# Kernel optimization log

Measured on AMD Instinct MI355X. Metric: run time of the kernel, lower is better.

Reference implementation:

```python
import jax, jax.numpy as jnp
import numpy as np

LAYERS = [3, 256, 256, 256, 256, 256, 256, 3]
W_BC, W_DIV, W_JXB = 1.0, 1.0, 1.0  # weight1 = [1.0, 1.0, 1.0]


def setup_inputs() -> dict:
    key = jax.random.key(0)
    ks = jax.random.split(key, 32)
    N0, NF = 16384, 32768
    inp = {
        "x0": jax.random.uniform(ks[0], (N0, 1), jnp.float32),
        "y0": jax.random.uniform(ks[1], (N0, 1), jnp.float32),
        "bx0": jax.random.normal(ks[2], (N0, 1), jnp.float32),
        "by0": jax.random.normal(ks[3], (N0, 1), jnp.float32),
        "bz0": jax.random.normal(ks[4], (N0, 1), jnp.float32),
        "xyz_f": jax.random.uniform(ks[5], (NF, 3), jnp.float32),
        "lb": jnp.zeros((3,), jnp.float32),
        "ub": jnp.ones((3,), jnp.float32),
    }
    # Xavier-normal weights, zero biases (as in initialize_NN)
    for l in range(len(LAYERS) - 1):
        fan_in, fan_out = LAYERS[l], LAYERS[l + 1]
        std = (2.0 / (fan_in + fan_out)) ** 0.5
        inp[f"W{l}"] = std * jax.random.normal(ks[6 + l], (fan_in, fan_out), jnp.float32)
        inp[f"b{l}"] = jnp.zeros((1, fan_out), jnp.float32)
    return inp


def reference(x0, y0, bx0, by0, bz0, xyz_f, lb, ub,
              W0, b0, W1, b1, W2, b2, W3, b3, W4, b4, W5, b5, W6, b6):
    Ws = [W0, W1, W2, W3, W4, W5, W6]
    bs = [b0, b1, b2, b3, b4, b5, b6]

    def net(p):  # p: (3,) -> (3,) field [bx, by, bz]
        h = 2.0 * (p - lb) / (ub - lb) - 1.0
        for W, b in zip(Ws[:-1], bs[:-1]):
            h = jnp.tanh(h @ W + b[0])
        return h @ Ws[-1] + bs[-1][0]

    # Boundary term at z = 0
    pts0 = jnp.concatenate([x0, y0, jnp.zeros_like(x0)], axis=1)  # (N0, 3)
    b_bc = jax.vmap(net)(pts0)  # (N0, 3)

    # One fused forward-mode pass gives the full 3x3 Jacobian + primal,
    # replacing the 9 separate autograd.grad sweeps of the torch code.
    def val_and_jac(p):
        primal, jac = jax.vmap(lambda t: jax.jvp(net, (p,), (t,)))(jnp.eye(3, dtype=p.dtype))
        return primal[0], jac  # jac[j, i] = d b_i / d x_j

    bf, jac = jax.vmap(val_and_jac)(xyz_f)  # (NF, 3), (NF, 3, 3)

    div = jac[:, 0, 0] + jac[:, 1, 1] + jac[:, 2, 2]  # bx_x + by_y + bz_z
    bx, by, bz = bf[:, 0], bf[:, 1], bf[:, 2]
    jx = jac[:, 1, 2] - jac[:, 2, 1]  # bz_y - by_z
    jy = jac[:, 2, 0] - jac[:, 0, 2]  # bx_z - bz_x
    jz = jac[:, 0, 1] - jac[:, 1, 0]  # by_x - bx_y
    jxb = (jy * bz - jz * by) ** 2 + (jz * bx - jx * bz) ** 2 + (jx * by - jy * bx) ** 2

    loss = (W_BC * jnp.mean((b_bc[:, 0:1] - bx0) ** 2)
            + W_BC * jnp.mean((b_bc[:, 1:2] - by0) ** 2)
            + W_BC * jnp.mean((b_bc[:, 2:3] - bz0) ** 2)
            + W_DIV * jnp.mean(div ** 2)
            + W_JXB * jnp.mean(jxb))
    return loss
```

## Files before the change

kernel.cpp:

```cpp
#include <hip/hip_runtime.h>
#include <math.h>

typedef short bf16x8 __attribute__((ext_vector_type(8)));
typedef short bf16x4 __attribute__((ext_vector_type(4)));
typedef float f32x4 __attribute__((ext_vector_type(4)));

#define NPT0 16384
#define NPTF 32768

__device__ __forceinline__ short f2b(float f) {
  union { float f; unsigned u; } v; v.f = f;
  return (short)((v.u + 0x7FFFu + ((v.u >> 16) & 1u)) >> 16);
}
__device__ __forceinline__ int cvtpk(float a, float b) {
  int r;
  asm("v_cvt_pk_bf16_f32 %0, %1, %2" : "=v"(r) : "v"(a), "v"(b));
  return r;
}
__device__ __forceinline__ float tanh_fast(float z) {
  const float e = __expf(2.f * z);
  return 1.f - 2.f * __builtin_amdgcn_rcpf(e + 1.f);
}


__global__ void prep_kernel(const float* __restrict__ W1, const float* __restrict__ W2,
                            const float* __restrict__ W3, const float* __restrict__ W4,
                            const float* __restrict__ W5, const float* __restrict__ W6,
                            short* __restrict__ Wt)
{
  const int i = blockIdx.x * 256 + threadIdx.x;
  if (i < 5 * 65536) {
    const int layer = i >> 16;
    const float* src = layer == 0 ? W1 : layer == 1 ? W2 : layer == 2 ? W3
                     : layer == 3 ? W4 : W5;
    const int w  = i & 65535;
    const int nt = w >> 12;
    const int ks = (w >> 9) & 7;
    const int l  = (w >> 3) & 63;
    const int e  = w & 7;
    const int n  = nt * 16 + (l & 15);
    const int k  = ks * 32 + (l >> 4) * 8 + e;
    Wt[i] = f2b(src[k * 256 + n]);
  } else {
    const int w  = i - 5 * 65536;
    const int ks = w >> 9;
    const int l  = (w >> 3) & 63;
    const int e  = w & 7;
    const int n  = l & 15;
    const int k  = ks * 32 + (l >> 4) * 8 + e;
    Wt[i] = (n < 3) ? f2b(W6[k * 3 + n]) : (short)0;
  }
}

__global__ __launch_bounds__(256, 3) void field_kernel(
    const float* __restrict__ xyz_f,
    const float* __restrict__ lb, const float* __restrict__ ub,
    const float* __restrict__ W0, const float* __restrict__ b0,
    const float* __restrict__ b1, const float* __restrict__ b2,
    const float* __restrict__ b3, const float* __restrict__ b4,
    const float* __restrict__ b5,
    const short* __restrict__ Wt,
    const float* __restrict__ b6,
    float* __restrict__ part_div2, float* __restrict__ part_jxb)
{
  __shared__ short act[4 * 4096];
  __shared__ float redD[192];
  const int tid = threadIdx.x;
  const int lane = tid & 63;
  const int wv = tid >> 6;
  const int c = lane & 15;
  const int kg = lane >> 4;
  const int nbase = wv * 64;

  const float lbx = lb[0], lby = lb[1], lbz = lb[2];
  const float sx = 2.f / (ub[0] - lbx);
  const float sy = 2.f / (ub[1] - lby);
  const float sz = 2.f / (ub[2] - lbz);

  {
    const int p = tid >> 4;
    const int pt = blockIdx.x * 16 + p;
    const int n0 = (tid & 15) * 16;
    const float hx = (xyz_f[pt * 3 + 0] - lbx) * sx - 1.f;
    const float hy = (xyz_f[pt * 3 + 1] - lby) * sy - 1.f;
    const float hz = (xyz_f[pt * 3 + 2] - lbz) * sz - 1.f;
    float th[16], vx[16], vy[16], vz[16];
#pragma unroll
    for (int j = 0; j < 16; ++j) {
      const int n = n0 + j;
      const float w0 = W0[n], w1 = W0[256 + n], w2 = W0[512 + n];
      const float z = b0[n] + hx * w0 + hy * w1 + hz * w2;
      const float t = tanh_fast(z);
      const float g = 1.f - t * t;
      th[j] = t;
      vx[j] = g * sx * w0;
      vy[j] = g * sy * w1;
      vz[j] = g * sz * w2;
    }
    const int ks0 = n0 >> 5;
    const int kgb = (n0 >> 3) & 3;
#pragma unroll
    for (int half = 0; half < 2; ++half) {
      const int j0 = half * 8;
      const int idx = ks0 * 512 + ((kgb + half) * 16 + p) * 8;
      int4 o0, o1, o2, o3;
      o0.x = cvtpk(th[j0+0], th[j0+1]); o0.y = cvtpk(th[j0+2], th[j0+3]);
      o0.z = cvtpk(th[j0+4], th[j0+5]); o0.w = cvtpk(th[j0+6], th[j0+7]);
      o1.x = cvtpk(vx[j0+0], vx[j0+1]); o1.y = cvtpk(vx[j0+2], vx[j0+3]);
      o1.z = cvtpk(vx[j0+4], vx[j0+5]); o1.w = cvtpk(vx[j0+6], vx[j0+7]);
      o2.x = cvtpk(vy[j0+0], vy[j0+1]); o2.y = cvtpk(vy[j0+2], vy[j0+3]);
      o2.z = cvtpk(vy[j0+4], vy[j0+5]); o2.w = cvtpk(vy[j0+6], vy[j0+7]);
      o3.x = cvtpk(vz[j0+0], vz[j0+1]); o3.y = cvtpk(vz[j0+2], vz[j0+3]);
      o3.z = cvtpk(vz[j0+4], vz[j0+5]); o3.w = cvtpk(vz[j0+6], vz[j0+7]);
      *(int4*)&act[idx]          = o0;
      *(int4*)&act[4096 + idx]   = o1;
      *(int4*)&act[8192 + idx]   = o2;
      *(int4*)&act[12288 + idx]  = o3;
    }
  }
  __syncthreads();

  const float* const bsArr[5] = {b1, b2, b3, b4, b5};

#pragma unroll
  for (int layer = 0; layer < 5; ++layer) {
    const short* wt0 = Wt + layer * 65536 + wv * 4 * 4096 + lane * 8;
    const short* wt1 = wt0 + 4096;
    const short* wt2 = wt0 + 8192;
    const short* wt3 = wt0 + 12288;

    f32x4 acc[4][4];
#pragma unroll
    for (int s = 0; s < 4; ++s)
#pragma unroll
      for (int t = 0; t < 4; ++t) acc[s][t] = (f32x4){0.f, 0.f, 0.f, 0.f};

#pragma unroll
    for (int ks = 0; ks < 8; ++ks) {
      const int sa = ks * 512 + lane * 8;
      const bf16x8 a0 = *(const bf16x8*)&act[sa];
      const bf16x8 a1 = *(const bf16x8*)&act[4096 + sa];
      const bf16x8 a2 = *(const bf16x8*)&act[8192 + sa];
      const bf16x8 a3 = *(const bf16x8*)&act[12288 + sa];
      const bf16x8 w0 = *(const bf16x8*)(wt0 + ks * 512);
      const bf16x8 w1 = *(const bf16x8*)(wt1 + ks * 512);
      const bf16x8 w2 = *(const bf16x8*)(wt2 + ks * 512);
      const bf16x8 w3 = *(const bf16x8*)(wt3 + ks * 512);
      acc[0][0] = __builtin_amdgcn_mfma_f32_16x16x32_bf16(w0, a0, acc[0][0], 0, 0, 0);
      acc[1][0] = __builtin_amdgcn_mfma_f32_16x16x32_bf16(w0, a1, acc[1][0], 0, 0, 0);
      acc[2][0] = __builtin_amdgcn_mfma_f32_16x16x32_bf16(w0, a2, acc[2][0], 0, 0, 0);
      acc[3][0] = __builtin_amdgcn_mfma_f32_16x16x32_bf16(w0, a3, acc[3][0], 0, 0, 0);
      acc[0][1] = __builtin_amdgcn_mfma_f32_16x16x32_bf16(w1, a0, acc[0][1], 0, 0, 0);
      acc[1][1] = __builtin_amdgcn_mfma_f32_16x16x32_bf16(w1, a1, acc[1][1], 0, 0, 0);
      acc[2][1] = __builtin_amdgcn_mfma_f32_16x16x32_bf16(w1, a2, acc[2][1], 0, 0, 0);
      acc[3][1] = __builtin_amdgcn_mfma_f32_16x16x32_bf16(w1, a3, acc[3][1], 0, 0, 0);
      acc[0][2] = __builtin_amdgcn_mfma_f32_16x16x32_bf16(w2, a0, acc[0][2], 0, 0, 0);
      acc[1][2] = __builtin_amdgcn_mfma_f32_16x16x32_bf16(w2, a1, acc[1][2], 0, 0, 0);
      acc[2][2] = __builtin_amdgcn_mfma_f32_16x16x32_bf16(w2, a2, acc[2][2], 0, 0, 0);
      acc[3][2] = __builtin_amdgcn_mfma_f32_16x16x32_bf16(w2, a3, acc[3][2], 0, 0, 0);
      acc[0][3] = __builtin_amdgcn_mfma_f32_16x16x32_bf16(w3, a0, acc[0][3], 0, 0, 0);
      acc[1][3] = __builtin_amdgcn_mfma_f32_16x16x32_bf16(w3, a1, acc[1][3], 0, 0, 0);
      acc[2][3] = __builtin_amdgcn_mfma_f32_16x16x32_bf16(w3, a2, acc[2][3], 0, 0, 0);
      acc[3][3] = __builtin_amdgcn_mfma_f32_16x16x32_bf16(w3, a3, acc[3][3], 0, 0, 0);
    }
    __syncthreads();

    const float* bl = bsArr[layer];
#pragma unroll
    for (int t = 0; t < 4; ++t) {
      const int n0 = nbase + t * 16 + kg * 4;
      const f32x4 bias = *(const f32x4*)(bl + n0);
      float th[4], g[4];
#pragma unroll
      for (int r = 0; r < 4; ++r) {
        th[r] = tanh_fast(acc[0][t][r] + bias[r]);
        g[r] = 1.f - th[r] * th[r];
      }
      int2 o0, o1, o2, o3;
      o0.x = cvtpk(th[0], th[1]);
      o0.y = cvtpk(th[2], th[3]);
      o1.x = cvtpk(g[0] * acc[1][t][0], g[1] * acc[1][t][1]);
      o1.y = cvtpk(g[2] * acc[1][t][2], g[3] * acc[1][t][3]);
      o2.x = cvtpk(g[0] * acc[2][t][0], g[1] * acc[2][t][1]);
      o2.y = cvtpk(g[2] * acc[2][t][2], g[3] * acc[2][t][3]);
      o3.x = cvtpk(g[0] * acc[3][t][0], g[1] * acc[3][t][1]);
      o3.y = cvtpk(g[2] * acc[3][t][2], g[3] * acc[3][t][3]);
      const int idx = (n0 >> 5) * 512 + (((n0 >> 3) & 3) * 16 + c) * 8 + (n0 & 7);
      *(int2*)&act[idx]         = o0;
      *(int2*)&act[4096 + idx]  = o1;
      *(int2*)&act[8192 + idx]  = o2;
      *(int2*)&act[12288 + idx] = o3;
    }
    __syncthreads();
  }

  {
    const short* w6 = Wt + 5 * 65536 + lane * 8;
    f32x4 accT = (f32x4){0.f, 0.f, 0.f, 0.f};
#pragma unroll
    for (int ks = 0; ks < 8; ++ks) {
      const bf16x8 w = *(const bf16x8*)(w6 + ks * 512);
      const bf16x8 b = *(const bf16x8*)&act[wv * 4096 + ks * 512 + lane * 8];
      accT = __builtin_amdgcn_mfma_f32_16x16x32_bf16(w, b, accT, 0, 0, 0);
    }
    if (kg == 0) {
      redD[wv * 48 + 0  + c] = accT[0];
      redD[wv * 48 + 16 + c] = accT[1];
      redD[wv * 48 + 32 + c] = accT[2];
    }
  }
  __syncthreads();
  if (tid < 16) {
    const int p = tid;
    const float bx = redD[0 + p]  + b6[0];
    const float by = redD[16 + p] + b6[1];
    const float bz = redD[32 + p] + b6[2];
    const float j00 = redD[48 + p],  j01 = redD[64 + p],  j02 = redD[80 + p];
    const float j10 = redD[96 + p],  j11 = redD[112 + p], j12 = redD[128 + p];
    const float j20 = redD[144 + p], j21 = redD[160 + p], j22 = redD[176 + p];
    const float dv = j00 + j11 + j22;
    const float jx = j12 - j21;
    const float jy = j20 - j02;
    const float jz = j01 - j10;
    const float e1 = jy * bz - jz * by;
    const float e2 = jz * bx - jx * bz;
    const float e3 = jx * by - jy * bx;
    float d2 = dv * dv;
    float jb = e1 * e1 + e2 * e2 + e3 * e3;
#pragma unroll
    for (int m = 1; m < 16; m <<= 1) {
      d2 += __shfl_xor(d2, m);
      jb += __shfl_xor(jb, m);
    }
    if (tid == 0) {
      part_div2[blockIdx.x] = d2;
      part_jxb[blockIdx.x]  = jb;
    }
  }
}

__global__ __launch_bounds__(256, 4) void bc_kernel(
    const float* __restrict__ x0, const float* __restrict__ y0,
    const float* __restrict__ bx0, const float* __restrict__ by0,
    const float* __restrict__ bz0,
    const float* __restrict__ lb, const float* __restrict__ ub,
    const float* __restrict__ W0, const float* __restrict__ b0,
    const float* __restrict__ b1, const float* __restrict__ b2,
    const float* __restrict__ b3, const float* __restrict__ b4,
    const float* __restrict__ b5,
    const short* __restrict__ Wt,
    const float* __restrict__ b6,
    float* __restrict__ part_bc)
{
  __shared__ short act[4096];
  const int tid = threadIdx.x;
  const int lane = tid & 63;
  const int wv = tid >> 6;
  const int c = lane & 15;
  const int kg = lane >> 4;
  const int nbase = wv * 64;

  const float lbx = lb[0], lby = lb[1], lbz = lb[2];
  const float sx = 2.f / (ub[0] - lbx);
  const float sy = 2.f / (ub[1] - lby);
  const float sz = 2.f / (ub[2] - lbz);

  {
    const int p = tid >> 4;
    const int pt = blockIdx.x * 16 + p;
    const int n0 = (tid & 15) * 16;
    const float hx = (x0[pt] - lbx) * sx - 1.f;
    const float hy = (y0[pt] - lby) * sy - 1.f;
    const float hz = (0.f - lbz) * sz - 1.f;
    float th[16];
#pragma unroll
    for (int j = 0; j < 16; ++j) {
      const int n = n0 + j;
      const float z = b0[n] + hx * W0[n] + hy * W0[256 + n] + hz * W0[512 + n];
      th[j] = tanh_fast(z);
    }
    const int ks0 = n0 >> 5;
    const int kgb = (n0 >> 3) & 3;
#pragma unroll
    for (int half = 0; half < 2; ++half) {
      const int j0 = half * 8;
      int4 o;
      o.x = cvtpk(th[j0+0], th[j0+1]); o.y = cvtpk(th[j0+2], th[j0+3]);
      o.z = cvtpk(th[j0+4], th[j0+5]); o.w = cvtpk(th[j0+6], th[j0+7]);
      *(int4*)&act[ks0 * 512 + ((kgb + half) * 16 + p) * 8] = o;
    }
  }
  __syncthreads();

  const float* const bsArr[5] = {b1, b2, b3, b4, b5};

#pragma unroll
  for (int layer = 0; layer < 5; ++layer) {
    const short* wt0 = Wt + layer * 65536 + wv * 4 * 4096 + lane * 8;

    bf16x8 a[8];
#pragma unroll
    for (int ks = 0; ks < 8; ++ks) a[ks] = *(const bf16x8*)&act[ks * 512 + lane * 8];
    __syncthreads();

    f32x4 acc[4];
#pragma unroll
    for (int t = 0; t < 4; ++t) acc[t] = (f32x4){0.f, 0.f, 0.f, 0.f};

#pragma unroll
    for (int ks = 0; ks < 8; ++ks) {
#pragma unroll
      for (int t = 0; t < 4; ++t) {
        const bf16x8 w = *(const bf16x8*)(wt0 + t * 4096 + ks * 512);
        acc[t] = __builtin_amdgcn_mfma_f32_16x16x32_bf16(w, a[ks], acc[t], 0, 0, 0);
      }
    }

    const float* bl = bsArr[layer];
#pragma unroll
    for (int t = 0; t < 4; ++t) {
      const int n0 = nbase + t * 16 + kg * 4;
      const f32x4 bias = *(const f32x4*)(bl + n0);
      float th[4];
#pragma unroll
      for (int r = 0; r < 4; ++r) th[r] = tanh_fast(acc[t][r] + bias[r]);
      int2 o;
      o.x = cvtpk(th[0], th[1]);
      o.y = cvtpk(th[2], th[3]);
      const int idx = (n0 >> 5) * 512 + (((n0 >> 3) & 3) * 16 + c) * 8 + (n0 & 7);
      *(int2*)&act[idx] = o;
    }
    __syncthreads();
  }

  if (wv == 0) {
    const short* w6 = Wt + 5 * 65536 + lane * 8;
    f32x4 accT = (f32x4){0.f, 0.f, 0.f, 0.f};
#pragma unroll
    for (int ks = 0; ks < 8; ++ks) {
      const bf16x8 w = *(const bf16x8*)(w6 + ks * 512);
      const bf16x8 b = *(const bf16x8*)&act[ks * 512 + lane * 8];
      accT = __builtin_amdgcn_mfma_f32_16x16x32_bf16(w, b, accT, 0, 0, 0);
    }
    if (lane < 16) {
      const int pt = blockIdx.x * 16 + lane;
      const float ex = accT[0] + b6[0] - bx0[pt];
      const float ey = accT[1] + b6[1] - by0[pt];
      const float ez = accT[2] + b6[2] - bz0[pt];
      float abc = ex * ex + ey * ey + ez * ez;
#pragma unroll
      for (int m = 1; m < 16; m <<= 1) abc += __shfl_xor(abc, m);
      if (lane == 0) part_bc[blockIdx.x] = abc;
    }
  }
}

__global__ void reduce_kernel(const float* __restrict__ parts, float* __restrict__ out)
{
  __shared__ float sdata[12];
  const int tid = threadIdx.x, lane = tid & 63, wv = tid >> 6;
  float d = 0.f, j = 0.f, b = 0.f;
  for (int i = tid; i < 2048; i += 256) { d += parts[i]; j += parts[2048 + i]; }
  for (int i = tid; i < 1024; i += 256) b += parts[4096 + i];
  for (int off = 32; off > 0; off >>= 1) {
    d += __shfl_down(d, off);
    j += __shfl_down(j, off);
    b += __shfl_down(b, off);
  }
  if (lane == 0) {
    sdata[wv * 3 + 0] = d;
    sdata[wv * 3 + 1] = j;
    sdata[wv * 3 + 2] = b;
  }
  __syncthreads();
  if (tid == 0) {
    float sd = 0.f, sj = 0.f, sb = 0.f;
    for (int w = 0; w < 4; ++w) {
      sd += sdata[w * 3 + 0];
      sj += sdata[w * 3 + 1];
      sb += sdata[w * 3 + 2];
    }
    out[0] = sb / (float)NPT0 + sd / (float)NPTF + sj / (float)NPTF;
  }
}

extern "C" void kernel_launch(void* const* d_in, const int* in_sizes, int n_in,
                              void* d_out, int out_size, void* d_ws, size_t ws_size,
                              hipStream_t stream)
{
  const float* x0    = (const float*)d_in[0];
  const float* y0    = (const float*)d_in[1];
  const float* bx0   = (const float*)d_in[2];
  const float* by0   = (const float*)d_in[3];
  const float* bz0   = (const float*)d_in[4];
  const float* xyz_f = (const float*)d_in[5];
  const float* lb    = (const float*)d_in[6];
  const float* ub    = (const float*)d_in[7];
  const float* W0 = (const float*)d_in[8];
  const float* b0 = (const float*)d_in[9];
  const float* W1 = (const float*)d_in[10];
  const float* b1 = (const float*)d_in[11];
  const float* W2 = (const float*)d_in[12];
  const float* b2 = (const float*)d_in[13];
  const float* W3 = (const float*)d_in[14];
  const float* b3 = (const float*)d_in[15];
  const float* W4 = (const float*)d_in[16];
  const float* b4 = (const float*)d_in[17];
  const float* W5 = (const float*)d_in[18];
  const float* b5 = (const float*)d_in[19];
  const float* W6 = (const float*)d_in[20];
  const float* b6 = (const float*)d_in[21];

  short* Wt = (short*)d_ws;
  float* parts = (float*)((char*)d_ws + (5 * 65536 + 4096) * sizeof(short));
  float* p_div2 = parts;
  float* p_jxb  = parts + 2048;
  float* p_bc   = parts + 4096;

  prep_kernel<<<1296, 256, 0, stream>>>(W1, W2, W3, W4, W5, W6, Wt);
  field_kernel<<<2048, 256, 0, stream>>>(xyz_f, lb, ub, W0, b0,
      b1, b2, b3, b4, b5, Wt, b6, p_div2, p_jxb);
  bc_kernel<<<1024, 256, 0, stream>>>(x0, y0, bx0, by0, bz0, lb, ub, W0, b0,
      b1, b2, b3, b4, b5, Wt, b6, p_bc);
  reduce_kernel<<<1, 256, 0, stream>>>(parts, (float*)d_out);
}
```

Measured before the change: 127.5 us.

## Process 32 points per block with 8 waves splitting output columns

Doubles each block to 512 threads and 32 points, with each of the 8 waves computing 2 output column tiles across two 16-point groups instead of 4 tiles for one group. Every weight fragment loaded from global memory now feeds twice as many MFMAs, halving weight traffic per point and the number of blocks. The cost is a doubled LDS activation buffer, a re-indexed tail reduction, and different occupancy and register-pressure behaviour under the new launch bounds.

```diff
diff --git a/kernel.cpp b/kernel.cpp
--- a/kernel.cpp
+++ b/kernel.cpp
@@ -2,7 +2,6 @@
 #include <math.h>
 
 typedef short bf16x8 __attribute__((ext_vector_type(8)));
-typedef short bf16x4 __attribute__((ext_vector_type(4)));
 typedef float f32x4 __attribute__((ext_vector_type(4)));
 
 #define NPT0 16384
@@ -21,7 +20,9 @@
   const float e = __expf(2.f * z);
   return 1.f - 2.f * __builtin_amdgcn_rcpf(e + 1.f);
 }
-
+__device__ __forceinline__ int inplane(int n, int c) {
+  return ((n >> 5) << 9) + ((((n >> 3) & 3) * 16 + c) << 3) + (n & 7);
+}
 
 __global__ void prep_kernel(const float* __restrict__ W1, const float* __restrict__ W2,
                             const float* __restrict__ W3, const float* __restrict__ W4,
@@ -52,7 +53,7 @@
   }
 }
 
-__global__ __launch_bounds__(256, 3) void field_kernel(
+__global__ __launch_bounds__(512, 4) void field_kernel(
     const float* __restrict__ xyz_f,
     const float* __restrict__ lb, const float* __restrict__ ub,
     const float* __restrict__ W0, const float* __restrict__ b0,
@@ -63,14 +64,13 @@
     const float* __restrict__ b6,
     float* __restrict__ part_div2, float* __restrict__ part_jxb)
 {
-  __shared__ short act[4 * 4096];
-  __shared__ float redD[192];
+  __shared__ short act[4 * 8192];
+  __shared__ float redD[4 * 96];
   const int tid = threadIdx.x;
   const int lane = tid & 63;
   const int wv = tid >> 6;
   const int c = lane & 15;
   const int kg = lane >> 4;
-  const int nbase = wv * 64;
 
   const float lbx = lb[0], lby = lb[1], lbz = lb[2];
   const float sx = 2.f / (ub[0] - lbx);
@@ -78,9 +78,10 @@
   const float sz = 2.f / (ub[2] - lbz);
 
   {
-    const int p = tid >> 4;
-    const int pt = blockIdx.x * 16 + p;
-    const int n0 = (tid & 15) * 16;
+    const int pp = tid & 15;
+    const int pg = (tid >> 4) & 1;
+    const int pt = blockIdx.x * 32 + pg * 16 + pp;
+    const int n0 = (tid >> 5) * 16;
     const float hx = (xyz_f[pt * 3 + 0] - lbx) * sx - 1.f;
     const float hy = (xyz_f[pt * 3 + 1] - lby) * sy - 1.f;
     const float hz = (xyz_f[pt * 3 + 2] - lbz) * sz - 1.f;
@@ -102,7 +103,7 @@
 #pragma unroll
     for (int half = 0; half < 2; ++half) {
       const int j0 = half * 8;
-      const int idx = ks0 * 512 + ((kgb + half) * 16 + p) * 8;
+      const int idx = pg * 4096 + ks0 * 512 + ((kgb + half) * 16 + pp) * 8;
       int4 o0, o1, o2, o3;
       o0.x = cvtpk(th[j0+0], th[j0+1]); o0.y = cvtpk(th[j0+2], th[j0+3]);
       o0.z = cvtpk(th[j0+4], th[j0+5]); o0.w = cvtpk(th[j0+6], th[j0+7]);
@@ -113,9 +114,9 @@
       o3.x = cvtpk(vz[j0+0], vz[j0+1]); o3.y = cvtpk(vz[j0+2], vz[j0+3]);
       o3.z = cvtpk(vz[j0+4], vz[j0+5]); o3.w = cvtpk(vz[j0+6], vz[j0+7]);
       *(int4*)&act[idx]          = o0;
-      *(int4*)&act[4096 + idx]   = o1;
-      *(int4*)&act[8192 + idx]   = o2;
-      *(int4*)&act[12288 + idx]  = o3;
+      *(int4*)&act[8192 + idx]   = o1;
+      *(int4*)&act[16384 + idx]  = o2;
+      *(int4*)&act[24576 + idx]  = o3;
     }
   }
   __syncthreads();
@@ -124,100 +125,96 @@
 
 #pragma unroll
   for (int layer = 0; layer < 5; ++layer) {
-    const short* wt0 = Wt + layer * 65536 + wv * 4 * 4096 + lane * 8;
-    const short* wt1 = wt0 + 4096;
-    const short* wt2 = wt0 + 8192;
-    const short* wt3 = wt0 + 12288;
-
-    f32x4 acc[4][4];
-#pragma unroll
-    for (int s = 0; s < 4; ++s)
-#pragma unroll
-      for (int t = 0; t < 4; ++t) acc[s][t] = (f32x4){0.f, 0.f, 0.f, 0.f};
+    const short* wbase = Wt + layer * 65536 + (wv * 2) * 4096 + lane * 8;
+
+    f32x4 acc[2][4][2];
+#pragma unroll
+    for (int t = 0; t < 2; ++t)
+#pragma unroll
+      for (int s = 0; s < 4; ++s)
+#pragma unroll
+        for (int g = 0; g < 2; ++g) acc[t][s][g] = (f32x4){0.f, 0.f, 0.f, 0.f};
 
 #pragma unroll
     for (int ks = 0; ks < 8; ++ks) {
       const int sa = ks * 512 + lane * 8;
-      const bf16x8 a0 = *(const bf16x8*)&act[sa];
-      const bf16x8 a1 = *(const bf16x8*)&act[4096 + sa];
-      const bf16x8 a2 = *(const bf16x8*)&act[8192 + sa];
-      const bf16x8 a3 = *(const bf16x8*)&act[12288 + sa];
-      const bf16x8 w0 = *(const bf16x8*)(wt0 + ks * 512);
-      const bf16x8 w1 = *(const bf16x8*)(wt1 + ks * 512);
-      const bf16x8 w2 = *(const bf16x8*)(wt2 + ks * 512);
-      const bf16x8 w3 = *(const bf16x8*)(wt3 + ks * 512);
-      acc[0][0] = __builtin_amdgcn_mfma_f32_16x16x32_bf16(w0, a0, acc[0][0], 0, 0, 0);
-      acc[1][0] = __builtin_amdgcn_mfma_f32_16x16x32_bf16(w0, a1, acc[1][0], 0, 0, 0);
-      acc[2][0] = __builtin_amdgcn_mfma_f32_16x16x32_bf16(w0, a2, acc[2][0], 0, 0, 0);
-      acc[3][0] = __builtin_amdgcn_mfma_f32_16x16x32_bf16(w0, a3, acc[3][0], 0, 0, 0);
-      acc[0][1] = __builtin_amdgcn_mfma_f32_16x16x32_bf16(w1, a0, acc[0][1], 0, 0, 0);
-      acc[1][1] = __builtin_amdgcn_mfma_f32_16x16x32_bf16(w1, a1, acc[1][1], 0, 0, 0);
-      acc[2][1] = __builtin_amdgcn_mfma_f32_16x16x32_bf16(w1, a2, acc[2][1], 0, 0, 0);
-      acc[3][1] = __builtin_amdgcn_mfma_f32_16x16x32_bf16(w1, a3, acc[3][1], 0, 0, 0);
-      acc[0][2] = __builtin_amdgcn_mfma_f32_16x16x32_bf16(w2, a0, acc[0][2], 0, 0, 0);
-      acc[1][2] = __builtin_amdgcn_mfma_f32_16x16x32_bf16(w2, a1, acc[1][2], 0, 0, 0);
-      acc[2][2] = __builtin_amdgcn_mfma_f32_16x16x32_bf16(w2, a2, acc[2][2], 0, 0, 0);
-      acc[3][2] = __builtin_amdgcn_mfma_f32_16x16x32_bf16(w2, a3, acc[3][2], 0, 0, 0);
-      acc[0][3] = __builtin_amdgcn_mfma_f32_16x16x32_bf16(w3, a0, acc[0][3], 0, 0, 0);
-      acc[1][3] = __builtin_amdgcn_mfma_f32_16x16x32_bf16(w3, a1, acc[1][3], 0, 0, 0);
-      acc[2][3] = __builtin_amdgcn_mfma_f32_16x16x32_bf16(w3, a2, acc[2][3], 0, 0, 0);
-      acc[3][3] = __builtin_amdgcn_mfma_f32_16x16x32_bf16(w3, a3, acc[3][3], 0, 0, 0);
+      const bf16x8 w0 = *(const bf16x8*)(wbase + ks * 512);
+      const bf16x8 w1 = *(const bf16x8*)(wbase + 4096 + ks * 512);
+#pragma unroll
+      for (int g = 0; g < 2; ++g) {
+        const bf16x8 a0 = *(const bf16x8*)&act[g * 4096 + sa];
+        const bf16x8 a1 = *(const bf16x8*)&act[8192 + g * 4096 + sa];
+        const bf16x8 a2 = *(const bf16x8*)&act[16384 + g * 4096 + sa];
+        const bf16x8 a3 = *(const bf16x8*)&act[24576 + g * 4096 + sa];
+        acc[0][0][g] = __builtin_amdgcn_mfma_f32_16x16x32_bf16(w0, a0, acc[0][0][g], 0, 0, 0);
+        acc[0][1][g] = __builtin_amdgcn_mfma_f32_16x16x32_bf16(w0, a1, acc[0][1][g], 0, 0, 0);
+        acc[0][2][g] = __builtin_amdgcn_mfma_f32_16x16x32_bf16(w0, a2, acc[0][2][g], 0, 0, 0);
+        acc[0][3][g] = __builtin_amdgcn_mfma_f32_16x16x32_bf16(w0, a3, acc[0][3][g], 0, 0, 0);
+        acc[1][0][g] = __builtin_amdgcn_mfma_f32_16x16x32_bf16(w1, a0, acc[1][0][g], 0, 0, 0);
+        acc[1][1][g] = __builtin_amdgcn_mfma_f32_16x16x32_bf16(w1, a1, acc[1][1][g], 0, 0, 0);
+        acc[1][2][g] = __builtin_amdgcn_mfma_f32_16x16x32_bf16(w1, a2, acc[1][2][g], 0, 0, 0);
+        acc[1][3][g] = __builtin_amdgcn_mfma_f32_16x16x32_bf16(w1, a3, acc[1][3][g], 0, 0, 0);
+      }
     }
     __syncthreads();
 
     const float* bl = bsArr[layer];
 #pragma unroll
-    for (int t = 0; t < 4; ++t) {
-      const int n0 = nbase + t * 16 + kg * 4;
+    for (int t = 0; t < 2; ++t) {
+      const int n0 = (wv * 2 + t) * 16 + kg * 4;
       const f32x4 bias = *(const f32x4*)(bl + n0);
-      float th[4], g[4];
-#pragma unroll
-      for (int r = 0; r < 4; ++r) {
-        th[r] = tanh_fast(acc[0][t][r] + bias[r]);
-        g[r] = 1.f - th[r] * th[r];
+#pragma unroll
+      for (int g = 0; g < 2; ++g) {
+        float th[4], gd[4];
+#pragma unroll
+        for (int r = 0; r < 4; ++r) {
+          th[r] = tanh_fast(acc[t][0][g][r] + bias[r]);
+          gd[r] = 1.f - th[r] * th[r];
+        }
+        int2 o0, o1, o2, o3;
+        o0.x = cvtpk(th[0], th[1]);
+        o0.y = cvtpk(th[2], th[3]);
+        o1.x = cvtpk(gd[0] * acc[t][1][g][0], gd[1] * acc[t][1][g][1]);
+        o1.y = cvtpk(gd[2] * acc[t][1][g][2], gd[3] * acc[t][1][g][3]);
+        o2.x = cvtpk(gd[0] * acc[t][2][g][0], gd[1] * acc[t][2][g][1]);
+        o2.y = cvtpk(gd[2] * acc[t][2][g][2], gd[3] * acc[t][2][g][3]);
+        o3.x = cvtpk(gd[0] * acc[t][3][g][0], gd[1] * acc[t][3][g][1]);
+        o3.y = cvtpk(gd[2] * acc[t][3][g][2], gd[3] * acc[t][3][g][3]);
+        const int idx = g * 4096 + inplane(n0, c);
+        *(int2*)&act[idx]          = o0;
+        *(int2*)&act[8192 + idx]   = o1;
+        *(int2*)&act[16384 + idx]  = o2;
+        *(int2*)&act[24576 + idx]  = o3;
       }
-      int2 o0, o1, o2, o3;
-      o0.x = cvtpk(th[0], th[1]);
-      o0.y = cvtpk(th[2], th[3]);
-      o1.x = cvtpk(g[0] * acc[1][t][0], g[1] * acc[1][t][1]);
-      o1.y = cvtpk(g[2] * acc[1][t][2], g[3] * acc[1][t][3]);
-      o2.x = cvtpk(g[0] * acc[2][t][0], g[1] * acc[2][t][1]);
-      o2.y = cvtpk(g[2] * acc[2][t][2], g[3] * acc[2][t][3]);
-      o3.x = cvtpk(g[0] * acc[3][t][0], g[1] * acc[3][t][1]);
-      o3.y = cvtpk(g[2] * acc[3][t][2], g[3] * acc[3][t][3]);
-      const int idx = (n0 >> 5) * 512 + (((n0 >> 3) & 3) * 16 + c) * 8 + (n0 & 7);
-      *(int2*)&act[idx]         = o0;
-      *(int2*)&act[4096 + idx]  = o1;
-      *(int2*)&act[8192 + idx]  = o2;
-      *(int2*)&act[12288 + idx] = o3;
     }
     __syncthreads();
   }
 
   {
+    const int s = wv >> 1, g = wv & 1;
     const short* w6 = Wt + 5 * 65536 + lane * 8;
     f32x4 accT = (f32x4){0.f, 0.f, 0.f, 0.f};
 #pragma unroll
     for (int ks = 0; ks < 8; ++ks) {
       const bf16x8 w = *(const bf16x8*)(w6 + ks * 512);
-      const bf16x8 b = *(const bf16x8*)&act[wv * 4096 + ks * 512 + lane * 8];
+      const bf16x8 b = *(const bf16x8*)&act[s * 8192 + g * 4096 + ks * 512 + lane * 8];
       accT = __builtin_amdgcn_mfma_f32_16x16x32_bf16(w, b, accT, 0, 0, 0);
     }
     if (kg == 0) {
-      redD[wv * 48 + 0  + c] = accT[0];
-      redD[wv * 48 + 16 + c] = accT[1];
-      redD[wv * 48 + 32 + c] = accT[2];
+      redD[s * 96 + 0  + g * 16 + c] = accT[0];
+      redD[s * 96 + 32 + g * 16 + c] = accT[1];
+      redD[s * 96 + 64 + g * 16 + c] = accT[2];
     }
   }
   __syncthreads();
-  if (tid < 16) {
+  if (tid < 32) {
     const int p = tid;
-    const float bx = redD[0 + p]  + b6[0];
-    const float by = redD[16 + p] + b6[1];
-    const float bz = redD[32 + p] + b6[2];
-    const float j00 = redD[48 + p],  j01 = redD[64 + p],  j02 = redD[80 + p];
-    const float j10 = redD[96 + p],  j11 = redD[112 + p], j12 = redD[128 + p];
-    const float j20 = redD[144 + p], j21 = redD[160 + p], j22 = redD[176 + p];
+    const float bx = redD[0 + p]   + b6[0];
+    const float by = redD[32 + p]  + b6[1];
+    const float bz = redD[64 + p]  + b6[2];
+    const float j00 = redD[96 + p],  j01 = redD[128 + p], j02 = redD[160 + p];
+    const float j10 = redD[192 + p], j11 = redD[224 + p], j12 = redD[256 + p];
+    const float j20 = redD[288 + p], j21 = redD[320 + p], j22 = redD[352 + p];
     const float dv = j00 + j11 + j22;
     const float jx = j12 - j21;
     const float jy = j20 - j02;
@@ -228,7 +225,7 @@
     float d2 = dv * dv;
     float jb = e1 * e1 + e2 * e2 + e3 * e3;
 #pragma unroll
-    for (int m = 1; m < 16; m <<= 1) {
+    for (int m = 1; m < 32; m <<= 1) {
       d2 += __shfl_xor(d2, m);
       jb += __shfl_xor(jb, m);
     }
@@ -239,7 +236,7 @@
   }
 }
 
-__global__ __launch_bounds__(256, 4) void bc_kernel(
+__global__ __launch_bounds__(512, 4) void bc_kernel(
     const float* __restrict__ x0, const float* __restrict__ y0,
     const float* __restrict__ bx0, const float* __restrict__ by0,
     const float* __restrict__ bz0,
@@ -252,13 +249,13 @@
     const float* __restrict__ b6,
     float* __restrict__ part_bc)
 {
-  __shared__ short act[4096];
+  __shared__ short act[8192];
+  __shared__ float red[2];
   const int tid = threadIdx.x;
   const int lane = tid & 63;
   const int wv = tid >> 6;
   const int c = lane & 15;
   const int kg = lane >> 4;
-  const int nbase = wv * 64;
 
   const float lbx = lb[0], lby = lb[1], lbz = lb[2];
   const float sx = 2.f / (ub[0] - lbx);
@@ -266,9 +263,10 @@
   const float sz = 2.f / (ub[2] - lbz);
 
   {
-    const int p = tid >> 4;
-    const int pt = blockIdx.x * 16 + p;
-    const int n0 = (tid & 15) * 16;
+    const int pp = tid & 15;
+    const int pg = (tid >> 4) & 1;
+    const int pt = blockIdx.x * 32 + pg * 16 + pp;
+    const int n0 = (tid >> 5) * 16;
     const float hx = (x0[pt] - lbx) * sx - 1.f;
     const float hy = (y0[pt] - lby) * sy - 1.f;
     const float hz = (0.f - lbz) * sz - 1.f;
@@ -287,7 +285,7 @@
       int4 o;
       o.x = cvtpk(th[j0+0], th[j0+1]); o.y = cvtpk(th[j0+2], th[j0+3]);
       o.z = cvtpk(th[j0+4], th[j0+5]); o.w = cvtpk(th[j0+6], th[j0+7]);
-      *(int4*)&act[ks0 * 512 + ((kgb + half) * 16 + p) * 8] = o;
+      *(int4*)&act[pg * 4096 + ks0 * 512 + ((kgb + half) * 16 + pp) * 8] = o;
     }
   }
   __syncthreads();
@@ -296,63 +294,74 @@
 
 #pragma unroll
   for (int layer = 0; layer < 5; ++layer) {
-    const short* wt0 = Wt + layer * 65536 + wv * 4 * 4096 + lane * 8;
-
-    bf16x8 a[8];
-#pragma unroll
-    for (int ks = 0; ks < 8; ++ks) a[ks] = *(const bf16x8*)&act[ks * 512 + lane * 8];
+    const short* wbase = Wt + layer * 65536 + (wv * 2) * 4096 + lane * 8;
+
+    bf16x8 a[2][8];
+#pragma unroll
+    for (int g = 0; g < 2; ++g)
+#pragma unroll
+      for (int ks = 0; ks < 8; ++ks)
+        a[g][ks] = *(const bf16x8*)&act[g * 4096 + ks * 512 + lane * 8];
     __syncthreads();
 
-    f32x4 acc[4];
-#pragma unroll
-    for (int t = 0; t < 4; ++t) acc[t] = (f32x4){0.f, 0.f, 0.f, 0.f};
+    f32x4 acc[2][2];
+#pragma unroll
+    for (int t = 0; t < 2; ++t)
+#pragma unroll
+      for (int g = 0; g < 2; ++g) acc[t][g] = (f32x4){0.f, 0.f, 0.f, 0.f};
 
 #pragma unroll
     for (int ks = 0; ks < 8; ++ks) {
-#pragma unroll
-      for (int t = 0; t < 4; ++t) {
-        const bf16x8 w = *(const bf16x8*)(wt0 + t * 4096 + ks * 512);
-        acc[t] = __builtin_amdgcn_mfma_f32_16x16x32_bf16(w, a[ks], acc[t], 0, 0, 0);
+      const bf16x8 w0 = *(const bf16x8*)(wbase + ks * 512);
+      const bf16x8 w1 = *(const bf16x8*)(wbase + 4096 + ks * 512);
+      acc[0][0] = __builtin_amdgcn_mfma_f32_16x16x32_bf16(w0, a[0][ks], acc[0][0], 0, 0, 0);
+      acc[0][1] = __builtin_amdgcn_mfma_f32_16x16x32_bf16(w0, a[1][ks], acc[0][1], 0, 0, 0);
+      acc[1][0] = __builtin_amdgcn_mfma_f32_16x16x32_bf16(w1, a[0][ks], acc[1][0], 0, 0, 0);
+      acc[1][1] = __builtin_amdgcn_mfma_f32_16x16x32_bf16(w1, a[1][ks], acc[1][1], 0, 0, 0);
+    }
+
+    const float* bl = bsArr[layer];
+#pragma unroll
+    for (int t = 0; t < 2; ++t) {
+      const int n0 = (wv * 2 + t) * 16 + kg * 4;
+      const f32x4 bias = *(const f32x4*)(bl + n0);
+#pragma unroll
+      for (int g = 0; g < 2; ++g) {
+        float th[4];
+#pragma unroll
+        for (int r = 0; r < 4; ++r) th[r] = tanh_fast(acc[t][g][r] + bias[r]);
+        int2 o;
+        o.x = cvtpk(th[0], th[1]);
+        o.y = cvtpk(th[2], th[3]);
+        *(int2*)&act[g * 4096 + inplane(n0, c)] = o;
       }
     }
-
-    const float* bl = bsArr[layer];
-#pragma unroll
-    for (int t = 0; t < 4; ++t) {
-      const int n0 = nbase + t * 16 + kg * 4;
-      const f32x4 bias = *(const f32x4*)(bl + n0);
-      float th[4];
-#pragma unroll
-      for (int r = 0; r < 4; ++r) th[r] = tanh_fast(acc[t][r] + bias[r]);
-      int2 o;
-      o.x = cvtpk(th[0], th[1]);
-      o.y = cvtpk(th[2], th[3]);
-      const int idx = (n0 >> 5) * 512 + (((n0 >> 3) & 3) * 16 + c) * 8 + (n0 & 7);
-      *(int2*)&act[idx] = o;
-    }
     __syncthreads();
   }
 
-  if (wv == 0) {
+  if (wv < 2) {
+    const int g = wv;
     const short* w6 = Wt + 5 * 65536 + lane * 8;
     f32x4 accT = (f32x4){0.f, 0.f, 0.f, 0.f};
 #pragma unroll
     for (int ks = 0; ks < 8; ++ks) {
       const bf16x8 w = *(const bf16x8*)(w6 + ks * 512);
-      const bf16x8 b = *(const bf16x8*)&act[ks * 512 + lane * 8];
+      const bf16x8 b = *(const bf16x8*)&act[g * 4096 + ks * 512 + lane * 8];
       accT = __builtin_amdgcn_mfma_f32_16x16x32_bf16(w, b, accT, 0, 0, 0);
     }
     if (lane < 16) {
-      const int pt = blockIdx.x * 16 + lane;
+      const int pt = blockIdx.x * 32 + g * 16 + lane;
       const float ex = accT[0] + b6[0] - bx0[pt];
       const float ey = accT[1] + b6[1] - by0[pt];
       const float ez = accT[2] + b6[2] - bz0[pt];
       float abc = ex * ex + ey * ey + ez * ez;
 #pragma unroll
       for (int m = 1; m < 16; m <<= 1) abc += __shfl_xor(abc, m);
-      if (lane == 0) part_bc[blockIdx.x] = abc;
-    }
-  }
+      if (lane == 0) red[g] = abc;
+    }
+  }
+  __syncthreads();
+  if (tid == 0) part_bc[blockIdx.x] = red[0] + red[1];
 }
 
 __global__ void reduce_kernel(const float* __restrict__ parts, float* __restrict__ out)
@@ -360,8 +369,8 @@
   __shared__ float sdata[12];
   const int tid = threadIdx.x, lane = tid & 63, wv = tid >> 6;
   float d = 0.f, j = 0.f, b = 0.f;
-  for (int i = tid; i < 2048; i += 256) { d += parts[i]; j += parts[2048 + i]; }
-  for (int i = tid; i < 1024; i += 256) b += parts[4096 + i];
+  for (int i = tid; i < 1024; i += 256) { d += parts[i]; j += parts[1024 + i]; }
+  for (int i = tid; i < 512; i += 256) b += parts[2048 + i];
   for (int off = 32; off > 0; off >>= 1) {
     d += __shfl_down(d, off);
     j += __shfl_down(j, off);
@@ -414,13 +423,13 @@
   short* Wt = (short*)d_ws;
   float* parts = (float*)((char*)d_ws + (5 * 65536 + 4096) * sizeof(short));
   float* p_div2 = parts;
-  float* p_jxb  = parts + 2048;
-  float* p_bc   = parts + 4096;
+  float* p_jxb  = parts + 1024;
+  float* p_bc   = parts + 2048;
 
   prep_kernel<<<1296, 256, 0, stream>>>(W1, W2, W3, W4, W5, W6, Wt);
-  field_kernel<<<2048, 256, 0, stream>>>(xyz_f, lb, ub, W0, b0,
+  field_kernel<<<1024, 512, 0, stream>>>(xyz_f, lb, ub, W0, b0,
       b1, b2, b3, b4, b5, Wt, b6, p_div2, p_jxb);
-  bc_kernel<<<1024, 256, 0, stream>>>(x0, y0, bx0, by0, bz0, lb, ub, W0, b0,
+  bc_kernel<<<512, 512, 0, stream>>>(x0, y0, bx0, by0, bz0, lb, ub, W0, b0,
       b1, b2, b3, b4, b5, Wt, b6, p_bc);
   reduce_kernel<<<1, 256, 0, stream>>>(parts, (float*)d_out);
 }
```

Measured after the change: 106.9 us. -16.1%, faster.
